# Kernel optimization log

Measured on AMD Instinct MI355X. Metric: run time of the kernel, lower is better.

## Reference

```python
import jax, jax.numpy as jnp
import numpy as np
from jax import lax

ITERS = 10
EPS = 1e-6
LOSS_WEIGHT = 1.0


def _max_pool3x3(x):
    # F.max_pool2d(x, kernel_size=3, stride=1, padding=1): torch pads with -inf for max pool
    return lax.reduce_window(x, -jnp.inf, lax.max,
                             window_dimensions=(1, 1, 3, 3),
                             window_strides=(1, 1, 1, 1),
                             padding=((0, 0), (0, 0), (1, 1), (1, 1)))


def _soft_erode(x):
    return -_max_pool3x3(-x)


def _soft_dilate(x):
    return _max_pool3x3(x)


def _soft_open(x):
    return _soft_dilate(_soft_erode(x))


def _soft_skel(img, iters):
    img = jnp.clip(img, 0.0, 1.0)
    img1 = _soft_open(img)
    skel = jax.nn.relu(img - img1)
    for _ in range(iters):
        img = _soft_erode(img)
        img1 = _soft_open(img)
        delta = jax.nn.relu(img - img1)
        skel = skel + jax.nn.relu(delta - skel * delta)
    return skel


def setup_inputs() -> dict:
    key = jax.random.key(0)
    k1, k2 = jax.random.split(key)
    B, C, H, W = 8, 2, 1024, 1024
    pred = jax.random.normal(k1, (B, C, H, W), dtype=jnp.float32)
    target = jax.random.uniform(k2, (B, C, H, W), dtype=jnp.float32)
    return {"pred": pred, "target": target}


def reference(pred, target):
    # sigmoid on logits
    p = jax.nn.sigmoid(pred)  # [B,C,H,W]
    t = target.astype(p.dtype)
    # per-class channel slicing is equivalent to channel-wise ops (pooling is per-channel)
    skel_p = _soft_skel(p, ITERS)
    skel_t = _soft_skel(t, ITERS)
    hw = (2, 3)
    tprec = jnp.sum(skel_p * t, axis=hw) / (jnp.sum(skel_p, axis=hw) + EPS)  # [B,C]
    tsens = jnp.sum(skel_t * p, axis=hw) / (jnp.sum(skel_t, axis=hw) + EPS)  # [B,C]
    cl_dice = 1.0 - 2.0 * tprec * tsens / (tprec + tsens + EPS)  # [B,C]
    # original: per-class mean over batch, then mean over classes == global mean
    return LOSS_WEIGHT * jnp.mean(cl_dice)
```

## Files before the change

kernel.cpp:

```cpp
#include <hip/hip_runtime.h>


#define TILE 64
#define HALO 12
#define RROWS 92
#define SD 52
#define IMG 1024
#define NBC 16
#define NITER 11
#define LEPS 1e-6f

typedef unsigned int u32;
typedef _Float16 hv2 __attribute__((ext_vector_type(2)));

struct __align__(16) U4 { u32 v[4]; };

__device__ __forceinline__ hv2 H2(u32 x) { union { u32 u; hv2 h; } c; c.u = x; return c.h; }
__device__ __forceinline__ u32 U2(hv2 x) { union { u32 u; hv2 h; } c; c.h = x; return c.u; }
__device__ __forceinline__ hv2 hmin2v(hv2 a, hv2 b) { return __builtin_elementwise_min(a, b); }
__device__ __forceinline__ hv2 hmax2v(hv2 a, hv2 b) { return __builtin_elementwise_max(a, b); }
__device__ __forceinline__ u32 dpp_prev16(u32 x) {
    return (u32)__builtin_amdgcn_update_dpp(0, (int)x, 0x101, 0xf, 0xf, true);
}
__device__ __forceinline__ u32 dpp_next16(u32 x) {
    return (u32)__builtin_amdgcn_update_dpp(0, (int)x, 0x111, 0xf, 0xf, true);
}
__device__ __forceinline__ u32 alignh(u32 hi, u32 lo) {
    return (u32)((((unsigned long long)hi << 32) | lo) >> 16);
}
__device__ __forceinline__ float sigmoidf(float x) { return 1.0f / (1.0f + __expf(-x)); }

template<bool IS_MIN>
__device__ __forceinline__ void hpass(const u32 d[4], u32 o[4]) {
    u32 dm = dpp_prev16(d[3]);
    u32 dp = dpp_next16(d[0]);
    u32 a[5];
    a[0] = alignh(d[0], dm);
    a[1] = alignh(d[1], d[0]);
    a[2] = alignh(d[2], d[1]);
    a[3] = alignh(d[3], d[2]);
    a[4] = alignh(dp,   d[3]);
#pragma unroll
    for (int q = 0; q < 4; ++q) {
        if (IS_MIN) o[q] = U2(hmin2v(hmin2v(H2(a[q]), H2(d[q])), H2(a[q + 1])));
        else        o[q] = U2(hmax2v(hmax2v(H2(a[q]), H2(d[q])), H2(a[q + 1])));
    }
}

__global__ __launch_bounds__(256, 4)
void skel_tile_kernel(const float* __restrict__ pred,
                      const float* __restrict__ target,
                      float* __restrict__ ws)
{
    __shared__ __align__(16) u32 bufA[RROWS * SD];
    __shared__ __align__(16) u32 bufB[RROWS * SD];

    const int tid = threadIdx.x;
    const int bc  = blockIdx.z & (NBC - 1);
    const int img = blockIdx.z >> 4;
    const int r0  = blockIdx.y * TILE;
    const int c0  = blockIdx.x * TILE;

    const float* src = (img == 0) ? pred : target;
    const size_t base = (size_t)bc * (size_t)(IMG * IMG);

    const bool edgeT = (blockIdx.y == 0);
    const bool edgeB = (blockIdx.y == 15);
    const bool edgeL = (blockIdx.x == 0);
    const bool edgeR = (blockIdx.x == 15);
    const int rdLo = edgeT ? 12 : 0;
    const int rdHi = edgeB ? 75 : (RROWS - 1);

    for (int t = tid; t < 88 * 12; t += 256) {
        int rr = t / 12;
        int g  = t - rr * 12;
        int gr = min(max(r0 + rr - HALO, 0), IMG - 1);
        const float* rowp = src + base + (size_t)gr * IMG;
        float f[8];
        int gc0 = c0 + 8 * g - HALO;
        if (g <= 10 && gc0 >= 0 && gc0 + 8 <= IMG) {
            float4 v0 = *(const float4*)(rowp + gc0);
            float4 v1 = *(const float4*)(rowp + gc0 + 4);
            f[0] = v0.x; f[1] = v0.y; f[2] = v0.z; f[3] = v0.w;
            f[4] = v1.x; f[5] = v1.y; f[6] = v1.z; f[7] = v1.w;
        } else {
#pragma unroll
            for (int i = 0; i < 8; ++i) {
                int rc = min(8 * g + i, 87);
                int gc = min(max(c0 + rc - HALO, 0), IMG - 1);
                f[i] = rowp[gc];
            }
        }
        U4 u;
#pragma unroll
        for (int q = 0; q < 4; ++q) {
            float a = f[2 * q], b = f[2 * q + 1];
            if (img == 0) { a = sigmoidf(a); b = sigmoidf(b); }
            else { a = fminf(fmaxf(a, 0.f), 1.f); b = fminf(fmaxf(b, 0.f), 1.f); }
            hv2 p; p[0] = (_Float16)a; p[1] = (_Float16)b;
            u.v[q] = U2(p);
        }
        *(uint4*)&bufA[rr * SD + 4 * g] = *(const uint4*)u.v;
    }

    const int strip = tid >> 4;
    const int g16   = tid & 15;
    const int coldw = 4 * min(g16, 11);
    const bool wact = (g16 < 12);

    const int rs_e = min(1 + 6 * strip, 85);
    const int rs_d = 12 + 4 * strip;

    u32 mk[4];
#pragma unroll
    for (int q = 0; q < 4; ++q) {
        int c = 8 * g16 + 2 * q;
        mk[q] = ((c >= 12 && c <= 75) ? 0xFFFFu : 0u) |
                ((c + 1 >= 12 && c + 1 <= 75) ? 0xFFFF0000u : 0u);
    }

    hv2 Sv[4][4];
#pragma unroll
    for (int j = 0; j < 4; ++j)
#pragma unroll
        for (int q = 0; q < 4; ++q) { Sv[j][q][0] = (_Float16)0; Sv[j][q][1] = (_Float16)0; }

    u32* cur = bufA;
    u32* oth = bufB;

    __syncthreads();

    for (int k = 0; k < NITER; ++k) {
        {
            U4 h[8];
            const u32* p = cur + (rs_e - 1) * SD + coldw;
#pragma unroll
            for (int j = 0; j < 8; ++j) {
                U4 u; *(uint4*)u.v = *(const uint4*)(p + j * SD);
                hpass<true>(u.v, h[j].v);
            }
            u32* q = oth + rs_e * SD + coldw;
#pragma unroll
            for (int j = 0; j < 6; ++j) {
                int row = rs_e + j;
                if (wact && row <= 86) {
                    U4 o;
#pragma unroll
                    for (int qd = 0; qd < 4; ++qd)
                        o.v[qd] = U2(hmin2v(hmin2v(H2(h[j].v[qd]), H2(h[j + 1].v[qd])),
                                            H2(h[j + 2].v[qd])));
                    *(uint4*)(q + j * SD) = *(const uint4*)o.v;
                }
            }
        }
        __syncthreads();

        {
            U4 w[6], m[6];
            if (!(edgeT || edgeB)) {
                const u32* p = oth + (rs_d - 1) * SD + coldw;
#pragma unroll
                for (int j = 0; j < 6; ++j)
                    *(uint4*)w[j].v = *(const uint4*)(p + j * SD);
            } else {
#pragma unroll
                for (int j = 0; j < 6; ++j) {
                    int rr = min(max(rs_d - 1 + j, rdLo), rdHi);
                    *(uint4*)w[j].v = *(const uint4*)(oth + rr * SD + coldw);
                }
            }
#pragma unroll
            for (int j = 0; j < 6; ++j) hpass<false>(w[j].v, m[j].v);

            if (edgeL && g16 == 1) {
#pragma unroll
                for (int j = 0; j < 6; ++j) {
                    u32 d2 = w[j].v[2];
                    u32 sw = (d2 >> 16) | (d2 << 16);
                    u32 pm = U2(hmax2v(H2(d2), H2(sw)));
                    m[j].v[2] = (m[j].v[2] & 0xFFFF0000u) | (pm & 0xFFFFu);
                }
            }
            if (edgeR && g16 == 9) {
#pragma unroll
                for (int j = 0; j < 6; ++j) {
                    u32 d1 = w[j].v[1];
                    u32 sw = (d1 >> 16) | (d1 << 16);
                    u32 pm = U2(hmax2v(H2(d1), H2(sw)));
                    m[j].v[1] = (m[j].v[1] & 0x0000FFFFu) | (pm & 0xFFFF0000u);
                }
            }

            const u32* pc = cur + rs_d * SD + coldw;
#pragma unroll
            for (int j = 0; j < 4; ++j) {
                U4 a; *(uint4*)a.v = *(const uint4*)(pc + j * SD);
#pragma unroll
                for (int qd = 0; qd < 4; ++qd) {
                    hv2 D = hmax2v(hmax2v(H2(m[j].v[qd]), H2(m[j + 1].v[qd])),
                                   H2(m[j + 2].v[qd]));
                    hv2 z; z[0] = (_Float16)0; z[1] = (_Float16)0;
                    hv2 d = hmax2v(H2(a.v[qd]) - D, z);
                    d = H2(U2(d) & mk[qd]);
                    hv2 s = Sv[j][qd];
                    hv2 t = hmax2v(d - s * d, z);
                    Sv[j][qd] = s + t;
                }
            }
        }

        { u32* t_ = cur; cur = oth; oth = t_; }
        __syncthreads();
    }

    const float* osrc = (img == 0) ? target : pred;
    float s_sum = 0.0f, sp_sum = 0.0f;
#pragma unroll
    for (int j = 0; j < 4; ++j) {
        int orow = r0 + 4 * strip + j;
#pragma unroll
        for (int q = 0; q < 4; ++q) {
#pragma unroll
            for (int e = 0; e < 2; ++e) {
                int rc = 8 * g16 + 2 * q + e;
                if (rc >= 12 && rc <= 75) {
                    float sv = (float)Sv[j][q][e];
                    float ov = osrc[base + (size_t)orow * IMG + (c0 + rc - HALO)];
                    if (img == 1) ov = sigmoidf(ov);
                    s_sum  += sv;
                    sp_sum += sv * ov;
                }
            }
        }
    }

#pragma unroll
    for (int off = 32; off > 0; off >>= 1) {
        s_sum  += __shfl_down(s_sum,  off, 64);
        sp_sum += __shfl_down(sp_sum, off, 64);
    }
    float* red = (float*)bufA;
    if ((tid & 63) == 0) {
        red[(tid >> 6) * 2 + 0] = sp_sum;
        red[(tid >> 6) * 2 + 1] = s_sum;
    }
    __syncthreads();
    if (tid == 0) {
        float a = (red[0] + red[2]) + (red[4] + red[6]);
        float b = (red[1] + red[3]) + (red[5] + red[7]);
        float* acc = ws + (size_t)blockIdx.z * 2;
        atomicAdd(acc + 0, a);
        atomicAdd(acc + 1, b);
    }
}

__global__ void finalize_kernel(const float* __restrict__ ws, float* __restrict__ out)
{
    if (threadIdx.x == 0) {
        float acc = 0.0f;
        for (int bc = 0; bc < NBC; ++bc) {
            float spt = ws[(0 * NBC + bc) * 2 + 0];
            float sp  = ws[(0 * NBC + bc) * 2 + 1];
            float stp = ws[(1 * NBC + bc) * 2 + 0];
            float st  = ws[(1 * NBC + bc) * 2 + 1];
            float tprec = spt / (sp + LEPS);
            float tsens = stp / (st + LEPS);
            acc += 1.0f - 2.0f * tprec * tsens / (tprec + tsens + LEPS);
        }
        out[0] = acc / (float)NBC;
    }
}

extern "C" void kernel_launch(void* const* d_in, const int* in_sizes, int n_in,
                              void* d_out, int out_size, void* d_ws, size_t ws_size,
                              hipStream_t stream) {
    const float* pred   = (const float*)d_in[0];
    const float* target = (const float*)d_in[1];
    float* ws  = (float*)d_ws;
    float* out = (float*)d_out;

    hipMemsetAsync(d_ws, 0, 2 * NBC * 2 * sizeof(float), stream);

    dim3 grid(IMG / TILE, IMG / TILE, 2 * NBC);
    skel_tile_kernel<<<grid, 256, 0, stream>>>(pred, target, ws);
    finalize_kernel<<<1, 64, 0, stream>>>(ws, out);
}
```

Measured before the change: 596.7 us.

## Shrink erosion range per iteration and do vertical-first separable min/max passes

Erosion now covers only the row range still needed at iteration k, which shrinks as the valid halo shrinks. Iterations are split into two template instantiations with 6 or 5 rows per strip. Both erode and dilate apply the vertical 3-tap first and then the horizontal pass, so fewer horizontal DPP passes run per output row. The column mask on delta is dropped and the shared buffer height is reduced. The unrolled loops save ALU and LDS traffic, but the shrinking ranges and edge clamps must still give correct halos.

```diff
diff --git a/kernel.cpp b/kernel.cpp
--- a/kernel.cpp
+++ b/kernel.cpp
@@ -3,7 +3,7 @@
 
 #define TILE 64
 #define HALO 12
-#define RROWS 92
+#define RROWS 88
 #define SD 52
 #define IMG 1024
 #define NBC 16
@@ -47,6 +47,96 @@
     }
 }
 
+template<int JMAX>
+__device__ __forceinline__ void iter_body(int k, u32* cur, u32* oth,
+        int strip, int g16, int coldw, bool wact, int rs_d,
+        bool edgeI, int rdLo, int rdHi, bool edgeL, bool edgeR,
+        hv2 (&Sv)[4][4])
+{
+    const int lo = min(k + 1, 11);
+    const int hi = max(86 - k, 76);
+    const int rs_e = min(lo + JMAX * strip, hi - (JMAX - 1));
+    {
+        const u32* p = cur + (rs_e - 1) * SD + coldw;
+        u32* qo = oth + rs_e * SD + coldw;
+        U4 r0, r1, r2;
+        *(uint4*)r0.v = *(const uint4*)(p);
+        *(uint4*)r1.v = *(const uint4*)(p + SD);
+#pragma unroll
+        for (int j = 0; j < JMAX; ++j) {
+            *(uint4*)r2.v = *(const uint4*)(p + (j + 2) * SD);
+            U4 vv, o;
+#pragma unroll
+            for (int q = 0; q < 4; ++q)
+                vv.v[q] = U2(hmin2v(hmin2v(H2(r0.v[q]), H2(r1.v[q])), H2(r2.v[q])));
+            hpass<true>(vv.v, o.v);
+            if (wact) *(uint4*)(qo + j * SD) = *(const uint4*)o.v;
+            r0 = r1; r1 = r2;
+        }
+    }
+    __syncthreads();
+
+    {
+        U4 w[6];
+        if (edgeI) {
+            const u32* p = oth + (rs_d - 1) * SD + coldw;
+#pragma unroll
+            for (int j = 0; j < 6; ++j)
+                *(uint4*)w[j].v = *(const uint4*)(p + j * SD);
+        } else {
+#pragma unroll
+            for (int j = 0; j < 6; ++j) {
+                int rr = min(max(rs_d - 1 + j, rdLo), rdHi);
+                *(uint4*)w[j].v = *(const uint4*)(oth + rr * SD + coldw);
+            }
+        }
+        U4 V[4], m[4];
+#pragma unroll
+        for (int i = 0; i < 4; ++i) {
+#pragma unroll
+            for (int q = 0; q < 4; ++q)
+                V[i].v[q] = U2(hmax2v(hmax2v(H2(w[i].v[q]), H2(w[i + 1].v[q])),
+                                      H2(w[i + 2].v[q])));
+            hpass<false>(V[i].v, m[i].v);
+        }
+
+        if (edgeL && g16 == 1) {
+#pragma unroll
+            for (int i = 0; i < 4; ++i) {
+                u32 d2 = V[i].v[2];
+                u32 sw = (d2 >> 16) | (d2 << 16);
+                u32 pm = U2(hmax2v(H2(d2), H2(sw)));
+                m[i].v[2] = (m[i].v[2] & 0xFFFF0000u) | (pm & 0xFFFFu);
+            }
+        }
+        if (edgeR && g16 == 9) {
+#pragma unroll
+            for (int i = 0; i < 4; ++i) {
+                u32 d1 = V[i].v[1];
+                u32 sw = (d1 >> 16) | (d1 << 16);
+                u32 pm = U2(hmax2v(H2(d1), H2(sw)));
+                m[i].v[1] = (m[i].v[1] & 0x0000FFFFu) | (pm & 0xFFFF0000u);
+            }
+        }
+
+        const u32* pc = cur + rs_d * SD + coldw;
+#pragma unroll
+        for (int i = 0; i < 4; ++i) {
+            U4 a; *(uint4*)a.v = *(const uint4*)(pc + i * SD);
+#pragma unroll
+            for (int qd = 0; qd < 4; ++qd) {
+                hv2 D = H2(m[i].v[qd]);
+                hv2 z; z[0] = (_Float16)0; z[1] = (_Float16)0;
+                hv2 d = hmax2v(H2(a.v[qd]) - D, z);
+                hv2 s = Sv[i][qd];
+                hv2 t = hmax2v(d - s * d, z);
+                Sv[i][qd] = s + t;
+            }
+        }
+    }
+    __syncthreads();
+}
+
 __global__ __launch_bounds__(256, 4)
 void skel_tile_kernel(const float* __restrict__ pred,
                       const float* __restrict__ target,
@@ -68,6 +158,7 @@
     const bool edgeB = (blockIdx.y == 15);
     const bool edgeL = (blockIdx.x == 0);
     const bool edgeR = (blockIdx.x == 15);
+    const bool edgeI = !(edgeT || edgeB);
     const int rdLo = edgeT ? 12 : 0;
     const int rdHi = edgeB ? 75 : (RROWS - 1);
 
@@ -108,16 +199,7 @@
     const int coldw = 4 * min(g16, 11);
     const bool wact = (g16 < 12);
 
-    const int rs_e = min(1 + 6 * strip, 85);
     const int rs_d = 12 + 4 * strip;
-
-    u32 mk[4];
-#pragma unroll
-    for (int q = 0; q < 4; ++q) {
-        int c = 8 * g16 + 2 * q;
-        mk[q] = ((c >= 12 && c <= 75) ? 0xFFFFu : 0u) |
-                ((c + 1 >= 12 && c + 1 <= 75) ? 0xFFFF0000u : 0u);
-    }
 
     hv2 Sv[4][4];
 #pragma unroll
@@ -130,87 +212,17 @@
 
     __syncthreads();
 
-    for (int k = 0; k < NITER; ++k) {
-        {
-            U4 h[8];
-            const u32* p = cur + (rs_e - 1) * SD + coldw;
-#pragma unroll
-            for (int j = 0; j < 8; ++j) {
-                U4 u; *(uint4*)u.v = *(const uint4*)(p + j * SD);
-                hpass<true>(u.v, h[j].v);
-            }
-            u32* q = oth + rs_e * SD + coldw;
-#pragma unroll
-            for (int j = 0; j < 6; ++j) {
-                int row = rs_e + j;
-                if (wact && row <= 86) {
-                    U4 o;
-#pragma unroll
-                    for (int qd = 0; qd < 4; ++qd)
-                        o.v[qd] = U2(hmin2v(hmin2v(H2(h[j].v[qd]), H2(h[j + 1].v[qd])),
-                                            H2(h[j + 2].v[qd])));
-                    *(uint4*)(q + j * SD) = *(const uint4*)o.v;
-                }
-            }
-        }
-        __syncthreads();
-
-        {
-            U4 w[6], m[6];
-            if (!(edgeT || edgeB)) {
-                const u32* p = oth + (rs_d - 1) * SD + coldw;
-#pragma unroll
-                for (int j = 0; j < 6; ++j)
-                    *(uint4*)w[j].v = *(const uint4*)(p + j * SD);
-            } else {
-#pragma unroll
-                for (int j = 0; j < 6; ++j) {
-                    int rr = min(max(rs_d - 1 + j, rdLo), rdHi);
-                    *(uint4*)w[j].v = *(const uint4*)(oth + rr * SD + coldw);
-                }
-            }
-#pragma unroll
-            for (int j = 0; j < 6; ++j) hpass<false>(w[j].v, m[j].v);
-
-            if (edgeL && g16 == 1) {
-#pragma unroll
-                for (int j = 0; j < 6; ++j) {
-                    u32 d2 = w[j].v[2];
-                    u32 sw = (d2 >> 16) | (d2 << 16);
-                    u32 pm = U2(hmax2v(H2(d2), H2(sw)));
-                    m[j].v[2] = (m[j].v[2] & 0xFFFF0000u) | (pm & 0xFFFFu);
-                }
-            }
-            if (edgeR && g16 == 9) {
-#pragma unroll
-                for (int j = 0; j < 6; ++j) {
-                    u32 d1 = w[j].v[1];
-                    u32 sw = (d1 >> 16) | (d1 << 16);
-                    u32 pm = U2(hmax2v(H2(d1), H2(sw)));
-                    m[j].v[1] = (m[j].v[1] & 0x0000FFFFu) | (pm & 0xFFFF0000u);
-                }
-            }
-
-            const u32* pc = cur + rs_d * SD + coldw;
-#pragma unroll
-            for (int j = 0; j < 4; ++j) {
-                U4 a; *(uint4*)a.v = *(const uint4*)(pc + j * SD);
-#pragma unroll
-                for (int qd = 0; qd < 4; ++qd) {
-                    hv2 D = hmax2v(hmax2v(H2(m[j].v[qd]), H2(m[j + 1].v[qd])),
-                                   H2(m[j + 2].v[qd]));
-                    hv2 z; z[0] = (_Float16)0; z[1] = (_Float16)0;
-                    hv2 d = hmax2v(H2(a.v[qd]) - D, z);
-                    d = H2(U2(d) & mk[qd]);
-                    hv2 s = Sv[j][qd];
-                    hv2 t = hmax2v(d - s * d, z);
-                    Sv[j][qd] = s + t;
-                }
-            }
-        }
-
-        { u32* t_ = cur; cur = oth; oth = t_; }
-        __syncthreads();
+#pragma unroll 1
+    for (int k = 0; k < 3; ++k) {
+        iter_body<6>(k, cur, oth, strip, g16, coldw, wact, rs_d,
+                     edgeI, rdLo, rdHi, edgeL, edgeR, Sv);
+        u32* t_ = cur; cur = oth; oth = t_;
+    }
+#pragma unroll 1
+    for (int k = 3; k < NITER; ++k) {
+        iter_body<5>(k, cur, oth, strip, g16, coldw, wact, rs_d,
+                     edgeI, rdLo, rdHi, edgeL, edgeR, Sv);
+        u32* t_ = cur; cur = oth; oth = t_;
     }
 
     const float* osrc = (img == 0) ? target : pred;
```

After: 499.4 us. -16.3%, faster.
